# Kernel optimization log

Hardware: AMD Instinct MI355X
Metric: run time of the kernel (lower is better)

The kernel has to match this reference:

```python
import jax, jax.numpy as jnp
import numpy as np

B, H, S = 128, 512, 2048

def setup_inputs() -> dict:
    key = jax.random.key(0)
    ks = jax.random.split(key, 8)
    sc = 1.0 / np.sqrt(H)
    return {
        "all_hidden": jax.random.normal(ks[0], (B, H, S), dtype=jnp.float32),
        "v_att": jax.random.normal(ks[1], (H,), dtype=jnp.float32) * sc,
        "W_att": jax.random.normal(ks[2], (H, H), dtype=jnp.float32) * sc,
        "v_ptr": jax.random.normal(ks[3], (H,), dtype=jnp.float32) * sc,
        "fc1_w": jax.random.normal(ks[4], (H, H), dtype=jnp.float32) * sc,
        "fc1_b": jax.random.normal(ks[5], (H,), dtype=jnp.float32) * sc,
        "fc2_w": jax.random.normal(ks[6], (H, H), dtype=jnp.float32) * sc,
        "fc2_b": jax.random.normal(ks[7], (H,), dtype=jnp.float32) * sc,
    }

def reference(all_hidden, v_att, W_att, v_ptr, fc1_w, fc1_b, fc2_w, fc2_b):
    # all_hidden: [B, H, S]
    # Attention: attns = softmax(v . tanh(W @ all_hidden), over seq)
    scores = jnp.einsum('hk,bks->bhs', W_att, all_hidden)          # [B,H,S]
    attn = jax.nn.softmax(jnp.einsum('h,bhs->bs', v_att, jnp.tanh(scores)), axis=-1)  # [B,S]
    # context = attn @ all_hidden^T  -> [B,H]
    context = jnp.einsum('bs,bhs->bh', attn, all_hidden)
    # 2-layer MLP with relu (torch Linear: x @ W^T + b)
    out = jax.nn.relu(context @ fc1_w.T + fc1_b)
    out = jax.nn.relu(out @ fc2_w.T + fc2_b)                        # [B,H]
    # probs = v . tanh(all_hidden + out broadcast over seq)
    probs = jnp.einsum('h,bhs->bs', v_ptr, jnp.tanh(all_hidden + out[:, :, None]))  # [B,S]
    return probs
```

## Files before the change

### kernel.cpp

```cpp
#include <hip/hip_runtime.h>
#include <hip/hip_bf16.h>

#define B_ 128
#define H_ 512
#define S_ 2048
#define ST 64
#define NP (S_/ST)

typedef short  bf16x8  __attribute__((ext_vector_type(8)));
typedef float  floatx4 __attribute__((ext_vector_type(4)));
typedef short  short4v __attribute__((ext_vector_type(4)));

#define KT_TANH 2.8853900817779268f

__device__ __forceinline__ unsigned short f2bf(float f){
  unsigned u = __float_as_uint(f);
  unsigned r = (u + 0x7fffu + ((u >> 16) & 1u)) >> 16;
  return (unsigned short)r;
}
__device__ __forceinline__ float bf2f(unsigned short h){
  return __uint_as_float(((unsigned)h) << 16);
}
__device__ __forceinline__ float tanh_r(float a){
  float e = __builtin_amdgcn_exp2f(a);
  return __builtin_amdgcn_rcpf(e + 1.f);
}
__device__ __forceinline__ int swz(int s, int c){
  return (c & 56) | ((c ^ s) & 7);
}

__global__ __launch_bounds__(256) void k_convW(const float* __restrict__ W,
                                               unsigned short* __restrict__ Wb){
  int i = (blockIdx.x * 256 + threadIdx.x) * 4;
  float4 v = *(const float4*)(W + i);
  short4v o;
  o[0] = (short)f2bf(v.x); o[1] = (short)f2bf(v.y);
  o[2] = (short)f2bf(v.z); o[3] = (short)f2bf(v.w);
  *(short4v*)(Wb + i) = o;
}

__global__ __launch_bounds__(512, 4) void k_pass1(
    const float* __restrict__ hidden, const float* __restrict__ v_att,
    const unsigned short* __restrict__ Wb,
    float* __restrict__ part_m, float* __restrict__ part_z,
    float* __restrict__ part_ctx)
{
  union __align__(16) SMem {
    unsigned short Bs[ST * 512];
    float pctx[8 * H_];
  };
  __shared__ SMem sm;
  __shared__ float vatt[H_];
  __shared__ float twav[8][ST];
  __shared__ float ts[ST];
  __shared__ float es[ST];
  __shared__ float sva_sh;

  const int tid = threadIdx.x;
  const int w = tid >> 6, l = tid & 63;
  const int p = blockIdx.x & (NP - 1);
  const int b = blockIdx.x >> 5;
  const int s0 = p * ST;

  vatt[tid] = v_att[tid];

  {
    const float* src0 = hidden + ((size_t)b * H_) * S_ + s0 + l;
    #pragma unroll
    for (int it = 0; it < 8; ++it){
      const int c = w + it * 8;
      const float* src = src0 + (size_t)(c * 8) * S_;
      bf16x8 pk;
      #pragma unroll
      for (int j = 0; j < 8; ++j)
        pk[j] = (short)f2bf(__builtin_nontemporal_load(src + (size_t)j * S_));
      *(bf16x8*)(&sm.Bs[l * 512 + swz(l, c) * 8]) = pk;
    }
  }
  __syncthreads();

  if (w == 0){
    float sv = 0.f;
    #pragma unroll
    for (int k = 0; k < 8; ++k) sv += vatt[l + 64 * k];
    sv += __shfl_xor(sv, 1);  sv += __shfl_xor(sv, 2);
    sv += __shfl_xor(sv, 4);  sv += __shfl_xor(sv, 8);
    sv += __shfl_xor(sv, 16); sv += __shfl_xor(sv, 32);
    if (l == 0) sva_sh = sv;
  }

  const int quad = l >> 4, l16 = l & 15;
  float tacc[4] = {0.f, 0.f, 0.f, 0.f};

  {
    floatx4 acc[4][4];
    #pragma unroll
    for (int ti = 0; ti < 4; ++ti)
      #pragma unroll
      for (int ss = 0; ss < 4; ++ss){
        floatx4 z4 = {0.f, 0.f, 0.f, 0.f};
        acc[ti][ss] = z4;
      }

    for (int k0 = 0; k0 < H_; k0 += 32){
      bf16x8 a[4];
      #pragma unroll
      for (int ti = 0; ti < 4; ++ti)
        a[ti] = *(const bf16x8*)(Wb + ((w * 4 + ti) * 16 + l16) * H_ + k0 + quad * 8);
      bf16x8 bb[4];
      #pragma unroll
      for (int ss = 0; ss < 4; ++ss){
        const int c = (k0 >> 3) + quad;
        bb[ss] = *(const bf16x8*)(&sm.Bs[(ss * 16 + l16) * 512 + swz(l16, c) * 8]);
      }
      #pragma unroll
      for (int ti = 0; ti < 4; ++ti)
        #pragma unroll
        for (int ss = 0; ss < 4; ++ss)
          acc[ti][ss] = __builtin_amdgcn_mfma_f32_16x16x32_bf16(a[ti], bb[ss], acc[ti][ss], 0, 0, 0);
    }

    #pragma unroll
    for (int ti = 0; ti < 4; ++ti){
      const int hbase = (w * 4 + ti) * 16 + quad * 4;
      #pragma unroll
      for (int r = 0; r < 4; ++r){
        float va = vatt[hbase + r];
        #pragma unroll
        for (int ss = 0; ss < 4; ++ss)
          tacc[ss] = fmaf(va, tanh_r(acc[ti][ss][r] * KT_TANH), tacc[ss]);
      }
    }
  }

  #pragma unroll
  for (int ss = 0; ss < 4; ++ss){
    tacc[ss] += __shfl_xor(tacc[ss], 16);
    tacc[ss] += __shfl_xor(tacc[ss], 32);
  }
  if (l < 16){
    #pragma unroll
    for (int ss = 0; ss < 4; ++ss) twav[w][ss * 16 + l] = tacc[ss];
  }
  __syncthreads();
  if (tid < ST){
    float a = 0.f;
    #pragma unroll
    for (int ww = 0; ww < 8; ++ww) a += twav[ww][tid];
    ts[tid] = sva_sh - 2.f * a;
  }
  __syncthreads();

  float m = -1e30f;
  for (int s = 0; s < ST; ++s) m = fmaxf(m, ts[s]);
  if (tid < ST) es[tid] = __expf(ts[tid] - m);
  __syncthreads();
  float z = 0.f;
  for (int s = 0; s < ST; ++s) z += es[s];

  const int pidx = b * NP + p;
  if (tid == 0){ part_m[pidx] = m; part_z[pidx] = z; }

  float a8[8] = {0.f,0.f,0.f,0.f,0.f,0.f,0.f,0.f};
  #pragma unroll
  for (int j = 0; j < 8; ++j){
    const int s = w * 8 + j;
    const float ez = es[s];
    bf16x8 v = *(const bf16x8*)(&sm.Bs[s * 512 + swz(s, l) * 8]);
    #pragma unroll
    for (int e = 0; e < 8; ++e)
      a8[e] = fmaf(ez, bf2f((unsigned short)v[e]), a8[e]);
  }
  __syncthreads();
  {
    floatx4 lo = {a8[0], a8[1], a8[2], a8[3]};
    floatx4 hi = {a8[4], a8[5], a8[6], a8[7]};
    *(floatx4*)(&sm.pctx[w * H_ + l * 8])     = lo;
    *(floatx4*)(&sm.pctx[w * H_ + l * 8 + 4]) = hi;
  }
  __syncthreads();
  {
    float a = 0.f;
    #pragma unroll
    for (int ww = 0; ww < 8; ++ww) a += sm.pctx[ww * H_ + tid];
    part_ctx[(size_t)pidx * H_ + tid] = a;
  }
}

__global__ __launch_bounds__(256) void k_mlp(
    const float* __restrict__ part_m, const float* __restrict__ part_z,
    const float* __restrict__ part_ctx,
    const float* __restrict__ fc1_w, const float* __restrict__ fc1_b,
    const float* __restrict__ fc2_w, const float* __restrict__ fc2_b,
    float* __restrict__ out2)
{
  __shared__ float ctx[H_];
  __shared__ float h1[H_];
  __shared__ float wp[NP];
  const int b = blockIdx.x, tid = threadIdx.x;

  float m = -1e30f;
  for (int pp = 0; pp < NP; ++pp) m = fmaxf(m, part_m[b * NP + pp]);
  if (tid < NP) wp[tid] = __expf(part_m[b * NP + tid] - m);
  __syncthreads();
  float z = 0.f;
  for (int pp = 0; pp < NP; ++pp) z += wp[pp] * part_z[b * NP + pp];
  float invz = 1.f / z;

  for (int h = tid; h < H_; h += 256){
    float a = 0.f;
    for (int pp = 0; pp < NP; ++pp) a += wp[pp] * part_ctx[(size_t)(b * NP + pp) * H_ + h];
    ctx[h] = a * invz;
  }
  __syncthreads();

  for (int i = tid; i < H_; i += 256){
    const float4* row = (const float4*)(fc1_w + (size_t)i * H_);
    float4 s4 = {0.f, 0.f, 0.f, 0.f};
    for (int j = 0; j < H_ / 4; ++j){
      float4 wv = row[j];
      s4.x += wv.x * ctx[4 * j];     s4.y += wv.y * ctx[4 * j + 1];
      s4.z += wv.z * ctx[4 * j + 2]; s4.w += wv.w * ctx[4 * j + 3];
    }
    h1[i] = fmaxf(fc1_b[i] + s4.x + s4.y + s4.z + s4.w, 0.f);
  }
  __syncthreads();

  for (int i = tid; i < H_; i += 256){
    const float4* row = (const float4*)(fc2_w + (size_t)i * H_);
    float4 s4 = {0.f, 0.f, 0.f, 0.f};
    for (int j = 0; j < H_ / 4; ++j){
      float4 wv = row[j];
      s4.x += wv.x * h1[4 * j];     s4.y += wv.y * h1[4 * j + 1];
      s4.z += wv.z * h1[4 * j + 2]; s4.w += wv.w * h1[4 * j + 3];
    }
    out2[(size_t)b * H_ + i] = fmaxf(fc2_b[i] + s4.x + s4.y + s4.z + s4.w, 0.f);
  }
}

__global__ __launch_bounds__(256) void k_probs(
    const float* __restrict__ hidden, const float* __restrict__ v_ptr,
    const float* __restrict__ out2, float* __restrict__ probs)
{
  __shared__ float vp[H_], ko[H_];
  __shared__ float svp_sh;
  const int b = blockIdx.y, c = blockIdx.x, tid = threadIdx.x;
  vp[tid]       = v_ptr[tid];
  vp[tid + 256] = v_ptr[tid + 256];
  ko[tid]       = KT_TANH * out2[(size_t)b * H_ + tid];
  ko[tid + 256] = KT_TANH * out2[(size_t)b * H_ + tid + 256];
  __syncthreads();
  if (tid < 64){
    float sv = 0.f;
    #pragma unroll
    for (int k = 0; k < 8; ++k) sv += vp[tid + 64 * k];
    sv += __shfl_xor(sv, 1);  sv += __shfl_xor(sv, 2);
    sv += __shfl_xor(sv, 4);  sv += __shfl_xor(sv, 8);
    sv += __shfl_xor(sv, 16); sv += __shfl_xor(sv, 32);
    if (tid == 0) svp_sh = sv;
  }
  __syncthreads();

  const int s = c * 512 + tid * 2;
  const float* base = hidden + (size_t)b * H_ * S_ + s;
  float a0 = 0.f, a1 = 0.f;
  const float kt = KT_TANH;
  #pragma unroll 8
  for (int h = 0; h < H_; ++h){
    float2 hv = *(const float2*)(base + (size_t)h * S_);
    float wv = vp[h], o = ko[h];
    a0 = fmaf(wv, tanh_r(fmaf(kt, hv.x, o)), a0);
    a1 = fmaf(wv, tanh_r(fmaf(kt, hv.y, o)), a1);
  }
  float svp = svp_sh;
  float2 r2 = { svp - 2.f * a0, svp - 2.f * a1 };
  *(float2*)(probs + (size_t)b * S_ + s) = r2;
}

extern "C" void kernel_launch(void* const* d_in, const int* in_sizes, int n_in,
                              void* d_out, int out_size, void* d_ws, size_t ws_size,
                              hipStream_t stream)
{
  const float* hidden = (const float*)d_in[0];
  const float* v_att  = (const float*)d_in[1];
  const float* W_att  = (const float*)d_in[2];
  const float* v_ptr  = (const float*)d_in[3];
  const float* fc1_w  = (const float*)d_in[4];
  const float* fc1_b  = (const float*)d_in[5];
  const float* fc2_w  = (const float*)d_in[6];
  const float* fc2_b  = (const float*)d_in[7];
  float* probs = (float*)d_out;

  char* ws = (char*)d_ws;
  unsigned short* Wb = (unsigned short*)ws;
  float* part_m   = (float*)(ws + (512u<<10));
  float* part_z   = (float*)(ws + (512u<<10) + (16u<<10));
  float* part_ctx = (float*)(ws + (512u<<10) + (32u<<10));
  float* out2     = (float*)(ws + (512u<<10) + (32u<<10) + (8u<<20));

  hipLaunchKernelGGL(k_convW, dim3(256), dim3(256), 0, stream, W_att, Wb);
  hipLaunchKernelGGL(k_pass1, dim3(B_ * NP), dim3(512), 0, stream,
                     hidden, v_att, Wb, part_m, part_z, part_ctx);
  hipLaunchKernelGGL(k_mlp, dim3(B_), dim3(256), 0, stream,
                     part_m, part_z, part_ctx, fc1_w, fc1_b, fc2_w, fc2_b, out2);
  hipLaunchKernelGGL(k_probs, dim3(S_ / 512, B_), dim3(256), 0, stream,
                     hidden, v_ptr, out2, probs);
}
```

Measured before the change: 1.060 ms.

## Double-buffer MFMA operand loads and use wave-level softmax reductions in pass1

The pass1 GEMM loop now double-buffers its W and shared-memory B fragments, so loads for the next k-slice are issued while MFMAs on the current slice run. The W prefetch starts before the first barrier. The softmax max and sum over the 64-position tile now run as wave shuffles in one wave, which removes two block barriers and the serial 64-element loops every thread ran. The partial-context shared-memory layout is remapped, apparently to avoid bank conflicts, and the pass3 h-loop unroll goes from 8 to 16. These changes raise register pressure, which may hurt occupancy at the declared launch bounds.

```diff
diff --git a/kernel.cpp b/kernel.cpp
--- a/kernel.cpp
+++ b/kernel.cpp
@@ -52,9 +52,7 @@
   __shared__ SMem sm;
   __shared__ float vatt[H_];
   __shared__ float twav[8][ST];
-  __shared__ float ts[ST];
   __shared__ float es[ST];
-  __shared__ float sva_sh;
 
   const int tid = threadIdx.x;
   const int w = tid >> 6, l = tid & 63;
@@ -77,21 +75,27 @@
       *(bf16x8*)(&sm.Bs[l * 512 + swz(l, c) * 8]) = pk;
     }
   }
-  __syncthreads();
-
+
+  const int quad = l >> 4, l16 = l & 15;
+
+  float sva = 0.f;
   if (w == 0){
-    float sv = 0.f;
-    #pragma unroll
-    for (int k = 0; k < 8; ++k) sv += vatt[l + 64 * k];
-    sv += __shfl_xor(sv, 1);  sv += __shfl_xor(sv, 2);
-    sv += __shfl_xor(sv, 4);  sv += __shfl_xor(sv, 8);
-    sv += __shfl_xor(sv, 16); sv += __shfl_xor(sv, 32);
-    if (l == 0) sva_sh = sv;
-  }
-
-  const int quad = l >> 4, l16 = l & 15;
+    #pragma unroll
+    for (int k = 0; k < 8; ++k) sva += v_att[l + 64 * k];
+    sva += __shfl_xor(sva, 1);  sva += __shfl_xor(sva, 2);
+    sva += __shfl_xor(sva, 4);  sva += __shfl_xor(sva, 8);
+    sva += __shfl_xor(sva, 16); sva += __shfl_xor(sva, 32);
+  }
+
+  const unsigned short* Wbase = Wb + (w * 4 * 16 + l16) * H_ + quad * 8;
+  bf16x8 a0[4], a1[4], b0[4], b1[4];
+  #pragma unroll
+  for (int ti = 0; ti < 4; ++ti)
+    a0[ti] = *(const bf16x8*)(Wbase + ti * 16 * H_ + 0);
+
+  __syncthreads();
+
   float tacc[4] = {0.f, 0.f, 0.f, 0.f};
-
   {
     floatx4 acc[4][4];
     #pragma unroll
@@ -102,22 +106,39 @@
         acc[ti][ss] = z4;
       }
 
-    for (int k0 = 0; k0 < H_; k0 += 32){
-      bf16x8 a[4];
+    #pragma unroll
+    for (int ss = 0; ss < 4; ++ss)
+      b0[ss] = *(const bf16x8*)(&sm.Bs[(ss * 16 + l16) * 512 + swz(l16, quad) * 8]);
+
+    #pragma unroll
+    for (int k0 = 0; k0 < H_; k0 += 64){
+      const int kA = k0 + 32;
       #pragma unroll
       for (int ti = 0; ti < 4; ++ti)
-        a[ti] = *(const bf16x8*)(Wb + ((w * 4 + ti) * 16 + l16) * H_ + k0 + quad * 8);
-      bf16x8 bb[4];
-      #pragma unroll
-      for (int ss = 0; ss < 4; ++ss){
-        const int c = (k0 >> 3) + quad;
-        bb[ss] = *(const bf16x8*)(&sm.Bs[(ss * 16 + l16) * 512 + swz(l16, c) * 8]);
+        a1[ti] = *(const bf16x8*)(Wbase + ti * 16 * H_ + kA);
+      #pragma unroll
+      for (int ss = 0; ss < 4; ++ss)
+        b1[ss] = *(const bf16x8*)(&sm.Bs[(ss * 16 + l16) * 512 + swz(l16, (kA >> 3) + quad) * 8]);
+      #pragma unroll
+      for (int ti = 0; ti < 4; ++ti)
+        #pragma unroll
+        for (int ss = 0; ss < 4; ++ss)
+          acc[ti][ss] = __builtin_amdgcn_mfma_f32_16x16x32_bf16(a0[ti], b0[ss], acc[ti][ss], 0, 0, 0);
+
+      if (k0 + 64 < H_){
+        const int kB = k0 + 64;
+        #pragma unroll
+        for (int ti = 0; ti < 4; ++ti)
+          a0[ti] = *(const bf16x8*)(Wbase + ti * 16 * H_ + kB);
+        #pragma unroll
+        for (int ss = 0; ss < 4; ++ss)
+          b0[ss] = *(const bf16x8*)(&sm.Bs[(ss * 16 + l16) * 512 + swz(l16, (kB >> 3) + quad) * 8]);
       }
       #pragma unroll
       for (int ti = 0; ti < 4; ++ti)
         #pragma unroll
         for (int ss = 0; ss < 4; ++ss)
-          acc[ti][ss] = __builtin_amdgcn_mfma_f32_16x16x32_bf16(a[ti], bb[ss], acc[ti][ss], 0, 0, 0);
+          acc[ti][ss] = __builtin_amdgcn_mfma_f32_16x16x32_bf16(a1[ti], b1[ss], acc[ti][ss], 0, 0, 0);
     }
 
     #pragma unroll
@@ -143,23 +164,26 @@
     for (int ss = 0; ss < 4; ++ss) twav[w][ss * 16 + l] = tacc[ss];
   }
   __syncthreads();
-  if (tid < ST){
+
+  const int pidx = b * NP + p;
+  if (w == 0){
     float a = 0.f;
     #pragma unroll
-    for (int ww = 0; ww < 8; ++ww) a += twav[ww][tid];
-    ts[tid] = sva_sh - 2.f * a;
-  }
-  __syncthreads();
-
-  float m = -1e30f;
-  for (int s = 0; s < ST; ++s) m = fmaxf(m, ts[s]);
-  if (tid < ST) es[tid] = __expf(ts[tid] - m);
-  __syncthreads();
-  float z = 0.f;
-  for (int s = 0; s < ST; ++s) z += es[s];
-
-  const int pidx = b * NP + p;
-  if (tid == 0){ part_m[pidx] = m; part_z[pidx] = z; }
+    for (int ww = 0; ww < 8; ++ww) a += twav[ww][l];
+    float t = sva - 2.f * a;
+    float m = t;
+    m = fmaxf(m, __shfl_xor(m, 1));  m = fmaxf(m, __shfl_xor(m, 2));
+    m = fmaxf(m, __shfl_xor(m, 4));  m = fmaxf(m, __shfl_xor(m, 8));
+    m = fmaxf(m, __shfl_xor(m, 16)); m = fmaxf(m, __shfl_xor(m, 32));
+    float e = __expf(t - m);
+    es[l] = e;
+    float z = e;
+    z += __shfl_xor(z, 1);  z += __shfl_xor(z, 2);
+    z += __shfl_xor(z, 4);  z += __shfl_xor(z, 8);
+    z += __shfl_xor(z, 16); z += __shfl_xor(z, 32);
+    if (l == 0){ part_m[pidx] = m; part_z[pidx] = z; }
+  }
+  __syncthreads();
 
   float a8[8] = {0.f,0.f,0.f,0.f,0.f,0.f,0.f,0.f};
   #pragma unroll
@@ -175,14 +199,15 @@
   {
     floatx4 lo = {a8[0], a8[1], a8[2], a8[3]};
     floatx4 hi = {a8[4], a8[5], a8[6], a8[7]};
-    *(floatx4*)(&sm.pctx[w * H_ + l * 8])     = lo;
-    *(floatx4*)(&sm.pctx[w * H_ + l * 8 + 4]) = hi;
+    *(floatx4*)(&sm.pctx[w * H_ + l * 4])       = lo;
+    *(floatx4*)(&sm.pctx[w * H_ + 256 + l * 4]) = hi;
   }
   __syncthreads();
   {
+    const int idx = ((tid >> 3) << 2) + (tid & 3) + ((tid & 4) << 6);
     float a = 0.f;
     #pragma unroll
-    for (int ww = 0; ww < 8; ++ww) a += sm.pctx[ww * H_ + tid];
+    for (int ww = 0; ww < 8; ++ww) a += sm.pctx[ww * H_ + idx];
     part_ctx[(size_t)pidx * H_ + tid] = a;
   }
 }
@@ -265,7 +290,7 @@
   const float* base = hidden + (size_t)b * H_ * S_ + s;
   float a0 = 0.f, a1 = 0.f;
   const float kt = KT_TANH;
-  #pragma unroll 8
+  #pragma unroll 16
   for (int h = 0; h < H_; ++h){
     float2 hv = *(const float2*)(base + (size_t)h * S_);
     float wv = vp[h], o = ko[h];
```

After: 1.083 ms. +2.2%, slower.
